# Performance work log

Measured on AMD Instinct MI355X. Metric: run time of the kernel, lower is better.

The kernel has to match this reference:

```python
import jax, jax.numpy as jnp
import numpy as np

NEG_INF = -1.0e9  # matches module's negativeInfinity buffer


def setup_inputs() -> dict:
    key = jax.random.key(0)
    k0, k1, k2, k3 = jax.random.split(key, 4)
    bs, h, dh, qsl, sl = 2048, 8, 32, 64, 64
    q = jax.random.normal(k0, (bs, h, dh, qsl, 1), dtype=jnp.float32)
    k = jax.random.normal(k1, (bs, h, dh, 1, sl), dtype=jnp.float32)
    v = jax.random.normal(k2, (bs, h, dh, sl), dtype=jnp.float32)
    mask = jnp.zeros((bs, 1, qsl, sl), dtype=bool)
    gamma = jnp.ones((h,), dtype=jnp.float32)   # qk_GBN gamma
    bias = jax.random.normal(k3, (h,), dtype=jnp.float32) * 0.01  # qk_GBN bias
    return {"q": q, "k": k, "v": v, "mask": mask, "gamma": gamma, "bias": bias}


def reference(q, k, v, mask, gamma, bias):
    # scores: elementwise q*k summed over head-dim -> [bs, h, qsl, sl]
    qk = (q * k).sum(axis=2)
    # qk_GBN eval path: running m=0, s=1 -> per-head affine
    qk = qk * gamma[None, :, None, None] + bias[None, :, None, None]
    qk = jnp.where(mask, NEG_INF, qk)
    v_weights = jax.nn.softmax(qk, axis=-1)
    v_weights = jnp.where(mask, 0.0, v_weights)
    # sigmoid gating of attention weights
    v_weights = v_weights * jax.nn.sigmoid(qk)
    # output = v @ v_weights^T -> [bs, h, dvh, qsl]
    out = jnp.einsum("bhds,bhqs->bhdq", v, v_weights)
    return out
```

## Files before the change

### kernel.cpp

```cpp
#include <hip/hip_runtime.h>

typedef __attribute__((ext_vector_type(4))) float  f32x4;
typedef __attribute__((ext_vector_type(8))) __bf16 bf16x8;
typedef __attribute__((ext_vector_type(4))) __bf16 bf16x4;

#define MFMA16(a, b, c) __builtin_amdgcn_mfma_f32_16x16x32_bf16((a), (b), (c), 0, 0, 0)

__global__ __launch_bounds__(256, 4)
void mha_fused(const float* __restrict__ qg, const float* __restrict__ kg,
               const float* __restrict__ vg, const unsigned char* __restrict__ maskg,
               const float* __restrict__ gammag, const float* __restrict__ biasg,
               float* __restrict__ outg)
{
    const int bh = blockIdx.x;
    const int b  = bh >> 3;
    const int h  = bh & 7;
    const int t  = threadIdx.x;

    __shared__ __bf16 sQh[64][40];
    __shared__ __bf16 sQl[64][40];
    __shared__ __bf16 sKh[64][40];
    __shared__ __bf16 sKl[64][40];
    __shared__ __bf16 sV [32][72];
    __shared__ __bf16 sW [64][72];
    __shared__ unsigned char sM[64][80];

    const float* qb = qg + (size_t)bh * 2048;
    const float* kb = kg + (size_t)bh * 2048;
    const float* vb = vg + (size_t)bh * 2048;
    const unsigned char* mb = maskg + (size_t)b * 4096;
    float* ob = outg + (size_t)bh * 2048;

    {
        const int i = t & 63;
        #pragma unroll
        for (int g = 0; g < 2; ++g) {
            const int d0 = ((t >> 6) + 4 * g) * 4;
            float a0 = qb[(d0 + 0) * 64 + i];
            float a1 = qb[(d0 + 1) * 64 + i];
            float a2 = qb[(d0 + 2) * 64 + i];
            float a3 = qb[(d0 + 3) * 64 + i];
            __bf16 h0 = (__bf16)a0, h1 = (__bf16)a1, h2 = (__bf16)a2, h3 = (__bf16)a3;
            *(bf16x4*)&sQh[i][d0] = (bf16x4){h0, h1, h2, h3};
            *(bf16x4*)&sQl[i][d0] = (bf16x4){(__bf16)(a0 - (float)h0), (__bf16)(a1 - (float)h1),
                                             (__bf16)(a2 - (float)h2), (__bf16)(a3 - (float)h3)};
            a0 = kb[(d0 + 0) * 64 + i];
            a1 = kb[(d0 + 1) * 64 + i];
            a2 = kb[(d0 + 2) * 64 + i];
            a3 = kb[(d0 + 3) * 64 + i];
            h0 = (__bf16)a0; h1 = (__bf16)a1; h2 = (__bf16)a2; h3 = (__bf16)a3;
            *(bf16x4*)&sKh[i][d0] = (bf16x4){h0, h1, h2, h3};
            *(bf16x4*)&sKl[i][d0] = (bf16x4){(__bf16)(a0 - (float)h0), (__bf16)(a1 - (float)h1),
                                             (__bf16)(a2 - (float)h2), (__bf16)(a3 - (float)h3)};
        }
    }
    {
        const int d = t >> 3, j0 = (t & 7) * 8;
        f32x4 x0 = *(const f32x4*)&vb[d * 64 + j0];
        f32x4 x1 = *(const f32x4*)&vb[d * 64 + j0 + 4];
        bf16x8 vv = {(__bf16)x0[0], (__bf16)x0[1], (__bf16)x0[2], (__bf16)x0[3],
                     (__bf16)x1[0], (__bf16)x1[1], (__bf16)x1[2], (__bf16)x1[3]};
        *(bf16x8*)&sV[d][j0] = vv;
    }
    {
        const int i = t >> 2, j0 = (t & 3) * 16;
        uint4 m4 = *(const uint4*)&mb[i * 64 + j0];
        *(uint4*)&sM[i][j0] = m4;
    }
    __syncthreads();

    const int w  = t >> 6;
    const int li = t & 15;
    const int hi = (t >> 4) & 3;
    const int i  = w * 16 + li;

    bf16x8 qh = *(bf16x8*)&sQh[i][hi * 8];
    bf16x8 ql = *(bf16x8*)&sQl[i][hi * 8];
    f32x4 acc[4];
    #pragma unroll
    for (int jt = 0; jt < 4; ++jt) {
        bf16x8 ah = *(bf16x8*)&sKh[jt * 16 + li][hi * 8];
        bf16x8 al = *(bf16x8*)&sKl[jt * 16 + li][hi * 8];
        f32x4 c = {0.f, 0.f, 0.f, 0.f};
        c = MFMA16(al, qh, c);
        c = MFMA16(ah, ql, c);
        c = MFMA16(ah, qh, c);
        acc[jt] = c;
    }

    const float ga = gammag[h], be = biasg[h];
    float s[16];
    #pragma unroll
    for (int jt = 0; jt < 4; ++jt) {
        const unsigned int mw = *(const unsigned int*)&sM[i][jt * 16 + hi * 4];
        #pragma unroll
        for (int r = 0; r < 4; ++r) {
            float x = acc[jt][r] * ga + be;
            if ((mw >> (8 * r)) & 0xffu) x = -1.0e9f;
            s[jt * 4 + r] = x;
        }
    }
    float m = s[0];
    #pragma unroll
    for (int e = 1; e < 16; ++e) m = fmaxf(m, s[e]);
    m = fmaxf(m, __shfl_xor(m, 16));
    m = fmaxf(m, __shfl_xor(m, 32));
    float p[16], sum = 0.f;
    #pragma unroll
    for (int e = 0; e < 16; ++e) { p[e] = __expf(s[e] - m); sum += p[e]; }
    sum += __shfl_xor(sum, 16);
    sum += __shfl_xor(sum, 32);
    const float inv = 1.0f / sum;

    #pragma unroll
    for (int jt = 0; jt < 4; ++jt) {
        __bf16 wv0, wv1, wv2, wv3;
        {
            const int e = jt * 4 + 0; float g = 1.0f / (1.0f + __expf(-s[e])); wv0 = (__bf16)(p[e] * inv * g);
        }
        {
            const int e = jt * 4 + 1; float g = 1.0f / (1.0f + __expf(-s[e])); wv1 = (__bf16)(p[e] * inv * g);
        }
        {
            const int e = jt * 4 + 2; float g = 1.0f / (1.0f + __expf(-s[e])); wv2 = (__bf16)(p[e] * inv * g);
        }
        {
            const int e = jt * 4 + 3; float g = 1.0f / (1.0f + __expf(-s[e])); wv3 = (__bf16)(p[e] * inv * g);
        }
        *(bf16x4*)&sW[i][jt * 16 + hi * 4] = (bf16x4){wv0, wv1, wv2, wv3};
    }

    f32x4 o0 = {0.f, 0.f, 0.f, 0.f};
    f32x4 o1 = {0.f, 0.f, 0.f, 0.f};
    #pragma unroll
    for (int kt = 0; kt < 2; ++kt) {
        bf16x8 wb = *(bf16x8*)&sW[i][kt * 32 + hi * 8];
        bf16x8 va = *(bf16x8*)&sV[li][kt * 32 + hi * 8];
        bf16x8 vc = *(bf16x8*)&sV[16 + li][kt * 32 + hi * 8];
        o0 = MFMA16(va, wb, o0);
        o1 = MFMA16(vc, wb, o1);
    }
    #pragma unroll
    for (int r = 0; r < 4; ++r) {
        ob[(hi * 4 + r) * 64 + i]      = o0[r];
        ob[(16 + hi * 4 + r) * 64 + i] = o1[r];
    }
}

extern "C" void kernel_launch(void* const* d_in, const int* in_sizes, int n_in,
                              void* d_out, int out_size, void* d_ws, size_t ws_size,
                              hipStream_t stream)
{
    const float* q = (const float*)d_in[0];
    const float* k = (const float*)d_in[1];
    const float* v = (const float*)d_in[2];
    const unsigned char* mask = (const unsigned char*)d_in[3];
    const float* gamma = (const float*)d_in[4];
    const float* bias  = (const float*)d_in[5];
    float* out = (float*)d_out;

    const int num_bh = in_sizes[0] / 2048;
    dim3 grid(num_bh), block(256);
    hipLaunchKernelGGL(mha_fused, grid, block, 0, stream,
                       q, k, v, mask, gamma, bias, out);
}
```

Measured before the change: 101.6 us.

## Keep Q, mask and softmax weights in registers; swizzle K LDS; remap blocks

Q is loaded straight into registers and split into bf16 hi/lo there, and the mask is read directly from global memory, so the Q and mask LDS buffers are gone. The softmax weights are no longer written to LDS and read back: the score MFMA output layout is permuted so the weights feed the PV MFMA directly from registers, and V is read with a matching k-permutation. K is written to LDS with an XOR swizzle, the occupancy hint rises to 8 blocks, and block IDs are remapped so consecutive blocks are spread across batches. Less LDS traffic and a smaller footprint should raise occupancy, but the uncoalesced direct Q and mask loads may cost global bandwidth.

```diff
diff --git a/kernel.cpp b/kernel.cpp
--- a/kernel.cpp
+++ b/kernel.cpp
@@ -6,24 +6,22 @@
 
 #define MFMA16(a, b, c) __builtin_amdgcn_mfma_f32_16x16x32_bf16((a), (b), (c), 0, 0, 0)
 
-__global__ __launch_bounds__(256, 4)
+__global__ __launch_bounds__(256, 8)
 void mha_fused(const float* __restrict__ qg, const float* __restrict__ kg,
                const float* __restrict__ vg, const unsigned char* __restrict__ maskg,
                const float* __restrict__ gammag, const float* __restrict__ biasg,
                float* __restrict__ outg)
 {
-    const int bh = blockIdx.x;
+    const int bid = blockIdx.x;
+    const int chunk = gridDim.x >> 3;
+    const int bh = (bid & 7) * chunk + (bid >> 3);
     const int b  = bh >> 3;
     const int h  = bh & 7;
     const int t  = threadIdx.x;
 
-    __shared__ __bf16 sQh[64][40];
-    __shared__ __bf16 sQl[64][40];
     __shared__ __bf16 sKh[64][40];
     __shared__ __bf16 sKl[64][40];
     __shared__ __bf16 sV [32][72];
-    __shared__ __bf16 sW [64][72];
-    __shared__ unsigned char sM[64][80];
 
     const float* qb = qg + (size_t)bh * 2048;
     const float* kb = kg + (size_t)bh * 2048;
@@ -31,28 +29,34 @@
     const unsigned char* mb = maskg + (size_t)b * 4096;
     float* ob = outg + (size_t)bh * 2048;
 
+    const int w  = t >> 6;
+    const int li = t & 15;
+    const int hi = (t >> 4) & 3;
+    const int i  = w * 16 + li;
+
+    float qv[8];
+    #pragma unroll
+    for (int e = 0; e < 8; ++e) qv[e] = qb[(hi * 8 + e) * 64 + i];
+    unsigned int mw[4];
+    #pragma unroll
+    for (int jt = 0; jt < 4; ++jt)
+        mw[jt] = *(const unsigned int*)&mb[i * 64 + jt * 16 + hi * 4];
+
     {
-        const int i = t & 63;
+        const int j = t & 63, sel = t >> 6;
+        float a[8];
         #pragma unroll
-        for (int g = 0; g < 2; ++g) {
-            const int d0 = ((t >> 6) + 4 * g) * 4;
-            float a0 = qb[(d0 + 0) * 64 + i];
-            float a1 = qb[(d0 + 1) * 64 + i];
-            float a2 = qb[(d0 + 2) * 64 + i];
-            float a3 = qb[(d0 + 3) * 64 + i];
-            __bf16 h0 = (__bf16)a0, h1 = (__bf16)a1, h2 = (__bf16)a2, h3 = (__bf16)a3;
-            *(bf16x4*)&sQh[i][d0] = (bf16x4){h0, h1, h2, h3};
-            *(bf16x4*)&sQl[i][d0] = (bf16x4){(__bf16)(a0 - (float)h0), (__bf16)(a1 - (float)h1),
-                                             (__bf16)(a2 - (float)h2), (__bf16)(a3 - (float)h3)};
-            a0 = kb[(d0 + 0) * 64 + i];
-            a1 = kb[(d0 + 1) * 64 + i];
-            a2 = kb[(d0 + 2) * 64 + i];
-            a3 = kb[(d0 + 3) * 64 + i];
-            h0 = (__bf16)a0; h1 = (__bf16)a1; h2 = (__bf16)a2; h3 = (__bf16)a3;
-            *(bf16x4*)&sKh[i][d0] = (bf16x4){h0, h1, h2, h3};
-            *(bf16x4*)&sKl[i][d0] = (bf16x4){(__bf16)(a0 - (float)h0), (__bf16)(a1 - (float)h1),
-                                             (__bf16)(a2 - (float)h2), (__bf16)(a3 - (float)h3)};
+        for (int e = 0; e < 8; ++e) a[e] = kb[(sel * 8 + e) * 64 + j];
+        bf16x8 h8, l8;
+        #pragma unroll
+        for (int e = 0; e < 8; ++e) {
+            __bf16 hh = (__bf16)a[e];
+            h8[e] = hh;
+            l8[e] = (__bf16)(a[e] - (float)hh);
         }
+        const int slot = sel ^ ((j >> 3) & 3);
+        *(bf16x8*)&sKh[j][slot * 8] = h8;
+        *(bf16x8*)&sKl[j][slot * 8] = l8;
     }
     {
         const int d = t >> 3, j0 = (t & 7) * 8;
@@ -62,44 +66,37 @@
                      (__bf16)x1[0], (__bf16)x1[1], (__bf16)x1[2], (__bf16)x1[3]};
         *(bf16x8*)&sV[d][j0] = vv;
     }
-    {
-        const int i = t >> 2, j0 = (t & 3) * 16;
-        uint4 m4 = *(const uint4*)&mb[i * 64 + j0];
-        *(uint4*)&sM[i][j0] = m4;
+
+    bf16x8 qh, ql;
+    #pragma unroll
+    for (int e = 0; e < 8; ++e) {
+        __bf16 hh = (__bf16)qv[e];
+        qh[e] = hh;
+        ql[e] = (__bf16)(qv[e] - (float)hh);
     }
+
     __syncthreads();
-
-    const int w  = t >> 6;
-    const int li = t & 15;
-    const int hi = (t >> 4) & 3;
-    const int i  = w * 16 + li;
-
-    bf16x8 qh = *(bf16x8*)&sQh[i][hi * 8];
-    bf16x8 ql = *(bf16x8*)&sQl[i][hi * 8];
-    f32x4 acc[4];
-    #pragma unroll
-    for (int jt = 0; jt < 4; ++jt) {
-        bf16x8 ah = *(bf16x8*)&sKh[jt * 16 + li][hi * 8];
-        bf16x8 al = *(bf16x8*)&sKl[jt * 16 + li][hi * 8];
-        f32x4 c = {0.f, 0.f, 0.f, 0.f};
-        c = MFMA16(al, qh, c);
-        c = MFMA16(ah, ql, c);
-        c = MFMA16(ah, qh, c);
-        acc[jt] = c;
-    }
 
     const float ga = gammag[h], be = biasg[h];
     float s[16];
     #pragma unroll
     for (int jt = 0; jt < 4; ++jt) {
-        const unsigned int mw = *(const unsigned int*)&sM[i][jt * 16 + hi * 4];
+        const int j = jt * 16 + li;
+        const int slot = hi ^ ((j >> 3) & 3);
+        bf16x8 ah = *(bf16x8*)&sKh[j][slot * 8];
+        bf16x8 al = *(bf16x8*)&sKl[j][slot * 8];
+        f32x4 c = {0.f, 0.f, 0.f, 0.f};
+        c = MFMA16(al, qh, c);
+        c = MFMA16(ah, ql, c);
+        c = MFMA16(ah, qh, c);
         #pragma unroll
         for (int r = 0; r < 4; ++r) {
-            float x = acc[jt][r] * ga + be;
-            if ((mw >> (8 * r)) & 0xffu) x = -1.0e9f;
+            float x = c[r] * ga + be;
+            if ((mw[jt] >> (8 * r)) & 0xffu) x = -1.0e9f;
             s[jt * 4 + r] = x;
         }
     }
+
     float m = s[0];
     #pragma unroll
     for (int e = 1; e < 16; ++e) m = fmaxf(m, s[e]);
@@ -112,31 +109,31 @@
     sum += __shfl_xor(sum, 32);
     const float inv = 1.0f / sum;
 
+    bf16x4 wv[4];
     #pragma unroll
     for (int jt = 0; jt < 4; ++jt) {
-        __bf16 wv0, wv1, wv2, wv3;
-        {
-            const int e = jt * 4 + 0; float g = 1.0f / (1.0f + __expf(-s[e])); wv0 = (__bf16)(p[e] * inv * g);
+        #pragma unroll
+        for (int r = 0; r < 4; ++r) {
+            const int e = jt * 4 + r;
+            const float g = 1.0f / (1.0f + __expf(-s[e]));
+            wv[jt][r] = (__bf16)(p[e] * inv * g);
         }
-        {
-            const int e = jt * 4 + 1; float g = 1.0f / (1.0f + __expf(-s[e])); wv1 = (__bf16)(p[e] * inv * g);
-        }
-        {
-            const int e = jt * 4 + 2; float g = 1.0f / (1.0f + __expf(-s[e])); wv2 = (__bf16)(p[e] * inv * g);
-        }
-        {
-            const int e = jt * 4 + 3; float g = 1.0f / (1.0f + __expf(-s[e])); wv3 = (__bf16)(p[e] * inv * g);
-        }
-        *(bf16x4*)&sW[i][jt * 16 + hi * 4] = (bf16x4){wv0, wv1, wv2, wv3};
     }
 
     f32x4 o0 = {0.f, 0.f, 0.f, 0.f};
     f32x4 o1 = {0.f, 0.f, 0.f, 0.f};
     #pragma unroll
     for (int kt = 0; kt < 2; ++kt) {
-        bf16x8 wb = *(bf16x8*)&sW[i][kt * 32 + hi * 8];
-        bf16x8 va = *(bf16x8*)&sV[li][kt * 32 + hi * 8];
-        bf16x8 vc = *(bf16x8*)&sV[16 + li][kt * 32 + hi * 8];
+        bf16x4 wlo = wv[2 * kt], whi = wv[2 * kt + 1];
+        bf16x8 wb = {wlo[0], wlo[1], wlo[2], wlo[3], whi[0], whi[1], whi[2], whi[3]};
+        const int c0 = kt * 32 + hi * 4;
+        const int c1 = kt * 32 + 16 + hi * 4;
+        bf16x4 a0l = *(const bf16x4*)&sV[li][c0];
+        bf16x4 a0h = *(const bf16x4*)&sV[li][c1];
+        bf16x8 va = {a0l[0], a0l[1], a0l[2], a0l[3], a0h[0], a0h[1], a0h[2], a0h[3]};
+        bf16x4 a1l = *(const bf16x4*)&sV[16 + li][c0];
+        bf16x4 a1h = *(const bf16x4*)&sV[16 + li][c1];
+        bf16x8 vc = {a1l[0], a1l[1], a1l[2], a1l[3], a1h[0], a1h[1], a1h[2], a1h[3]};
         o0 = MFMA16(va, wb, o0);
         o1 = MFMA16(vc, wb, o1);
     }
```

Result: slower. 110.0 us (+8.2%).
